# Optimization experiments

Measured on AMD Instinct MI355X. Metric: run time of the kernel, lower is better.

## Reference

```python
import jax, jax.numpy as jnp
import numpy as np

N = 100000   # nodes
E = 1600000  # edges
EL = 1000000 # label edges
F = 64       # node_features (== LSTM hidden)
S = 64       # second_features
C = 32       # num_classes


def setup_inputs() -> dict:
    key = jax.random.key(0)
    ks = jax.random.split(key, 11)
    sc = 0.05
    return {
        "x": jax.random.normal(ks[0], (N, F), jnp.float32),
        "edge_index": jax.random.randint(ks[1], (2, E), 0, N, jnp.int32),
        "edge_label_index": jax.random.randint(ks[2], (2, EL), 0, N, jnp.int32),
        "W_ih": jax.random.normal(ks[3], (4 * F, F), jnp.float32) * sc,
        "W_hh": jax.random.normal(ks[4], (4 * F, F), jnp.float32) * sc,
        "b_ih": jax.random.normal(ks[5], (4 * F,), jnp.float32) * sc,
        "b_hh": jax.random.normal(ks[6], (4 * F,), jnp.float32) * sc,
        "W1": jax.random.normal(ks[7], (F, S), jnp.float32) * sc,
        "b1": jnp.zeros((S,), jnp.float32),
        "W2": jax.random.normal(ks[8], (S, C), jnp.float32) * sc,
        "b2": jnp.zeros((C,), jnp.float32),
    }


def lstm_step(x, W_ih, W_hh, b_ih, b_hh):
    # seq_len == 1, h0 = c0 = 0, so W_hh contributes nothing but both biases apply.
    gates = x @ W_ih.T + b_ih + b_hh          # [N, 4F], PyTorch gate order i,f,g,o
    i, f, g, o = jnp.split(gates, 4, axis=-1)
    c = jax.nn.sigmoid(i) * jnp.tanh(g)
    return jax.nn.sigmoid(o) * jnp.tanh(c)    # [N, F]


def gcn_conv(h, W, b, row, col, n):
    # PyG GCNConv default: add self-loops, symmetric normalization.
    hw = h @ W                                 # [n, out]
    loop = jnp.arange(n, dtype=row.dtype)
    row_sl = jnp.concatenate([row, loop])
    col_sl = jnp.concatenate([col, loop])
    deg = jax.ops.segment_sum(jnp.ones_like(col_sl, jnp.float32), col_sl, num_segments=n)
    dinv = jnp.where(deg > 0, jax.lax.rsqrt(deg), 0.0)
    norm = dinv[row_sl] * dinv[col_sl]         # [E+n]
    msgs = hw[row_sl] * norm[:, None]          # gather + scale
    out = jax.ops.segment_sum(msgs, col_sl, num_segments=n)  # scatter-add
    return out + b


def reference(x, edge_index, edge_label_index, W_ih, W_hh, b_ih, b_hh, W1, b1, W2, b2):
    n = x.shape[0]
    row, col = edge_index[0], edge_index[1]
    h = lstm_step(x, W_ih, W_hh, b_ih, b_hh)
    h = jax.nn.relu(gcn_conv(h, W1, b1, row, col, n))
    z = gcn_conv(h, W2, b2, row, col, n)       # [n, C]
    src = z[edge_label_index[0]]
    dst = z[edge_label_index[1]]
    return jnp.sum(src * dst, axis=-1)         # [EL]
```

## Files before the change

kernel.cpp:

```cpp
#include <hip/hip_runtime.h>
#include <hip/hip_bf16.h>
#include <hip/hip_fp16.h>
#include <math.h>
#include <stdint.h>

#define NBSH 9
#define CH   4096

typedef _Float16 h2v  __attribute__((ext_vector_type(2)));
typedef _Float16 half8 __attribute__((ext_vector_type(8)));
typedef float    f32x4 __attribute__((ext_vector_type(4)));

__device__ __forceinline__ float fdot2_(unsigned a, unsigned b, float c) {
    return __builtin_amdgcn_fdot2(__builtin_bit_cast(h2v, a),
                                  __builtin_bit_cast(h2v, b), c, false);
}

__device__ __forceinline__ float2 h2f2_(unsigned u) {
    return __half22float2(__builtin_bit_cast(__half2, u));
}

__device__ __forceinline__ float fast_sigmoid(float x) {
    float t = __expf(x);
    return 1.0f - __builtin_amdgcn_rcpf(1.0f + t);
}
__device__ __forceinline__ float fast_tanh(float x) {
    float t = __expf(2.0f * x);
    return 1.0f - 2.0f * __builtin_amdgcn_rcpf(1.0f + t);
}

__global__ __launch_bounds__(256) void k_trh(
    const float* __restrict__ Wih, const float* __restrict__ W1,
    const float* __restrict__ bih, const float* __restrict__ bhh,
    uint4* __restrict__ B1tab, uint4* __restrict__ B2tab,
    float* __restrict__ bsum,
    const int* __restrict__ col, int* __restrict__ bdeg, int E, int nbuck)
{
    if (blockIdx.x < 9) {
        int t = blockIdx.x * 256 + threadIdx.x;
        if (t < 1536) {
            int e = t >> 6, l = t & 63;
            int tt = e >> 1, kh = e & 1;
            int gate = tt >> 2, tj = tt & 3;
            int j = 16 * tj + (l & 15);
            int rowb = (gate == 0) ? j : (gate == 1) ? (128 + j) : (192 + j);
            int kbase = kh * 32 + 8 * (l >> 4);
            _Float16 v[8];
#pragma unroll
            for (int jj = 0; jj < 8; jj++)
                v[jj] = (_Float16)Wih[rowb * 64 + kbase + jj];
            B1tab[t] = *reinterpret_cast<uint4*>(v);
        } else if (t < 2048) {
            int u = t - 1536;
            int e = u >> 6, l = u & 63;
            int tt = e >> 1, kh = e & 1;
            int s = 16 * tt + (l & 15);
            int kbase = kh * 32 + 8 * (l >> 4);
            _Float16 v[8];
#pragma unroll
            for (int jj = 0; jj < 8; jj++)
                v[jj] = (_Float16)W1[(kbase + jj) * 64 + s];
            B2tab[u] = *reinterpret_cast<uint4*>(v);
        } else if (t < 2240) {
            int c = t - 2048;
            int gate = c >> 6, j = c & 63;
            int rowb = (gate == 0) ? j : (gate == 1) ? (128 + j) : (192 + j);
            bsum[c] = bih[rowb] + bhh[rowb];
        }
        return;
    }
    __shared__ int cnt[256];
    cnt[threadIdx.x] = 0;
    __syncthreads();
    int base = (blockIdx.x - 9) * CH;
    int end  = base + CH; if (end > E) end = E;
    for (int t = base + (int)threadIdx.x; t < end; t += 256)
        atomicAdd(&cnt[col[t] >> NBSH], 1);
    __syncthreads();
    if ((int)threadIdx.x < nbuck && cnt[threadIdx.x] > 0)
        atomicAdd(&bdeg[threadIdx.x], cnt[threadIdx.x]);
}

__global__ __launch_bounds__(256) void k_bscan(const int* __restrict__ bdeg,
        int* __restrict__ boff, int* __restrict__ gcur, int nbuck, int E) {
    __shared__ int tmp[256];
    int tid = threadIdx.x;
    int v = (tid < nbuck) ? bdeg[tid] : 0;
    tmp[tid] = v;
    __syncthreads();
#pragma unroll
    for (int s = 1; s < 256; s <<= 1) {
        int t = (tid >= s) ? tmp[tid - s] : 0;
        __syncthreads();
        tmp[tid] += t;
        __syncthreads();
    }
    if (tid < nbuck) {
        int o = tmp[tid] - v;
        boff[tid] = o;
        gcur[tid * 16] = o;
    }
    if (tid == 0) boff[nbuck] = E;
}

__global__ __launch_bounds__(256) void k_binl(
    const int* __restrict__ row, const int* __restrict__ col,
    int* __restrict__ gcur, int2* __restrict__ ebuf, int E, int nbuck,
    int eblocks,
    const float* __restrict__ x, const uint4* __restrict__ B1tab,
    const uint4* __restrict__ B2tab, const float* __restrict__ bsum,
    __half* __restrict__ hw1, int n)
{
    __shared__ int pool[9216];
    if ((int)blockIdx.x < eblocks) {
        int* cnt  = pool;
        int* lofs = pool + 256;
        int* gbase = pool + 512;
        int* cur2 = pool + 768;
        int2* stage = (int2*)(pool + 1024);
        int tid  = threadIdx.x;
        int base = blockIdx.x * CH;
        int ned  = E - base; if (ned > CH) ned = CH;

        cnt[tid] = 0;
        __syncthreads();

        int r[16], c[16], b[16];
#pragma unroll
        for (int i = 0; i < 16; i++) {
            int idx = i * 256 + tid;
            if (idx < ned) {
                r[i] = row[base + idx];
                c[i] = col[base + idx];
                b[i] = c[i] >> NBSH;
                atomicAdd(&cnt[b[i]], 1);
            } else { r[i] = 0; c[i] = 0; b[i] = -1; }
        }
        __syncthreads();

        int v = cnt[tid];
        lofs[tid] = v;
        __syncthreads();
#pragma unroll
        for (int s = 1; s < 256; s <<= 1) {
            int t = (tid >= s) ? lofs[tid - s] : 0;
            __syncthreads();
            lofs[tid] += t;
            __syncthreads();
        }
        int excl = lofs[tid] - v;
        __syncthreads();
        lofs[tid] = excl;
        cur2[tid] = excl;
        if (tid < nbuck && v > 0)
            gbase[tid] = atomicAdd(&gcur[tid * 16], v);
        __syncthreads();

#pragma unroll
        for (int i = 0; i < 16; i++) {
            if (b[i] >= 0) {
                int p = atomicAdd(&cur2[b[i]], 1);
                stage[p] = make_int2(r[i], c[i]);
            }
        }
        __syncthreads();

        for (int i = tid; i < ned; i += 256) {
            int2 rc = stage[i];
            int bb = rc.y >> NBSH;
            ebuf[gbase[bb] + (i - lofs[bb])] = rc;
        }
        return;
    }

    _Float16* hsp = (_Float16*)pool;
    int wv   = threadIdx.x >> 6;
    int lane = threadIdx.x & 63;
    int nbase = (((int)blockIdx.x - eblocks) * 4 + wv) * 16;
    if (nbase >= n) return;
    int m16 = lane & 15, q = lane >> 4;
    _Float16* hs = hsp + wv * 1152;

    int node = nbase + m16; if (node >= n) node = n - 1;
    const float* xr = x + (size_t)node * 64 + 8 * q;
    half8 a0, a1;
#pragma unroll
    for (int jj = 0; jj < 8; jj++) a0[jj] = (_Float16)xr[jj];
#pragma unroll
    for (int jj = 0; jj < 8; jj++) a1[jj] = (_Float16)xr[32 + jj];

    f32x4 c1[12];
#pragma unroll
    for (int t = 0; t < 12; t++) {
        f32x4 acc = {0.f, 0.f, 0.f, 0.f};
        half8 b0 = __builtin_bit_cast(half8, B1tab[(t * 2 + 0) * 64 + lane]);
        half8 b1 = __builtin_bit_cast(half8, B1tab[(t * 2 + 1) * 64 + lane]);
        acc = __builtin_amdgcn_mfma_f32_16x16x32_f16(a0, b0, acc, 0, 0, 0);
        acc = __builtin_amdgcn_mfma_f32_16x16x32_f16(a1, b1, acc, 0, 0, 0);
        c1[t] = acc;
    }

#pragma unroll
    for (int tj = 0; tj < 4; tj++) {
        int j = 16 * tj + m16;
        float bi = bsum[j], bg = bsum[64 + j], bo = bsum[128 + j];
#pragma unroll
        for (int r = 0; r < 4; r++) {
            float gi = c1[tj][r]     + bi;
            float gg = c1[4 + tj][r] + bg;
            float go = c1[8 + tj][r] + bo;
            float cc = fast_sigmoid(gi) * fast_tanh(gg);
            float h  = fast_sigmoid(go) * fast_tanh(cc);
            hs[(q * 4 + r) * 72 + j] = (_Float16)h;
        }
    }

    half8 a20 = __builtin_bit_cast(half8,
        *reinterpret_cast<const uint4*>(&hs[m16 * 72 + 8 * q]));
    half8 a21 = __builtin_bit_cast(half8,
        *reinterpret_cast<const uint4*>(&hs[m16 * 72 + 32 + 8 * q]));

    f32x4 c2[4];
#pragma unroll
    for (int t = 0; t < 4; t++) {
        f32x4 acc = {0.f, 0.f, 0.f, 0.f};
        half8 b0 = __builtin_bit_cast(half8, B2tab[(t * 2 + 0) * 64 + lane]);
        half8 b1 = __builtin_bit_cast(half8, B2tab[(t * 2 + 1) * 64 + lane]);
        acc = __builtin_amdgcn_mfma_f32_16x16x32_f16(a20, b0, acc, 0, 0, 0);
        acc = __builtin_amdgcn_mfma_f32_16x16x32_f16(a21, b1, acc, 0, 0, 0);
        c2[t] = acc;
    }

#pragma unroll
    for (int t = 0; t < 4; t++) {
#pragma unroll
        for (int r = 0; r < 4; r++) {
            int nd = nbase + q * 4 + r;
            if (nd < n)
                hw1[(size_t)nd * 64 + 16 * t + m16] = __float2half(c2[t][r]);
        }
    }
}

__global__ __launch_bounds__(512) void k_csr(
    const int2* __restrict__ ebuf, const int* __restrict__ boff,
    int* __restrict__ off, float* __restrict__ dinv,
    int* __restrict__ nbr, int n, int nbuck, int E)
{
    __shared__ int cnt[512], lofs[512];
    int b   = blockIdx.x;
    int tid = threadIdx.x;
    int c0  = b << NBSH;
    int nn  = n - c0; if (nn > 512) nn = 512; if (nn < 0) nn = 0;
    int lo  = boff[b], hi = boff[b + 1];

    cnt[tid] = 0;
    __syncthreads();
    for (int t = lo + tid; t < hi; t += 512)
        atomicAdd(&cnt[ebuf[t].y & 511], 1);
    __syncthreads();

    int v = cnt[tid];
    lofs[tid] = v;
    __syncthreads();
#pragma unroll
    for (int s = 1; s < 512; s <<= 1) {
        int t = (tid >= s) ? lofs[tid - s] : 0;
        __syncthreads();
        lofs[tid] += t;
        __syncthreads();
    }
    int excl = lofs[tid] - v;
    __syncthreads();

    if (tid < nn) {
        off[c0 + tid]  = lo + excl;
        dinv[c0 + tid] = 1.0f / sqrtf((float)(v + 1));
    }
    if (b == nbuck - 1 && tid == 0) off[n] = E;

    cnt[tid] = excl;
    __syncthreads();
    for (int t = lo + tid; t < hi; t += 512) {
        int2 rc = ebuf[t];
        int p = atomicAdd(&cnt[rc.y & 511], 1);
        nbr[lo + p] = rc.x;
    }
}

__global__ __launch_bounds__(256) void k_pull64(
    const __half* __restrict__ hw, const int* __restrict__ off,
    const int* __restrict__ nbr, const float* __restrict__ dinv,
    const float* __restrict__ b1, __half* __restrict__ h1, int n)
{
    int w    = (blockIdx.x * 256 + threadIdx.x) >> 6;
    int lane = threadIdx.x & 63;
    int quad = lane >> 4;
    int fp   = lane & 15;
    if (w * 4 >= n) return;
    int node = w * 4 + quad;
    bool alive = node < n;
    int s = 0, e = 0;
    if (alive) { s = off[node]; e = off[node + 1]; }

    float s0x=0.f,s0y=0.f,s0z=0.f,s0w=0.f;
    float s1x=0.f,s1y=0.f,s1z=0.f,s1w=0.f;
    float s2x=0.f,s2y=0.f,s2z=0.f,s2w=0.f;
    float s3x=0.f,s3y=0.f,s3z=0.f,s3w=0.f;

    for (int base = s; base < e; base += 16) {
        int t = base + fp;
        int idx = 0; float wv = 0.f;
        if (t < e) { idx = nbr[t]; wv = dinv[idx]; }
        int cnt = e - base; if (cnt > 16) cnt = 16;

        int k = 0;
        for (; k + 4 <= cnt; k += 4) {
            int   r0 = __shfl(idx, k + 0, 16); float w0 = __shfl(wv, k + 0, 16);
            int   r1 = __shfl(idx, k + 1, 16); float w1 = __shfl(wv, k + 1, 16);
            int   r2 = __shfl(idx, k + 2, 16); float w2 = __shfl(wv, k + 2, 16);
            int   r3 = __shfl(idx, k + 3, 16); float w3 = __shfl(wv, k + 3, 16);
            uint2 u0 = reinterpret_cast<const uint2*>(hw + (size_t)r0 * 64)[fp];
            uint2 u1 = reinterpret_cast<const uint2*>(hw + (size_t)r1 * 64)[fp];
            uint2 u2 = reinterpret_cast<const uint2*>(hw + (size_t)r2 * 64)[fp];
            uint2 u3 = reinterpret_cast<const uint2*>(hw + (size_t)r3 * 64)[fp];
            float2 l0 = h2f2_(u0.x), h0 = h2f2_(u0.y);
            float2 l1 = h2f2_(u1.x), h1f = h2f2_(u1.y);
            float2 l2 = h2f2_(u2.x), h2 = h2f2_(u2.y);
            float2 l3 = h2f2_(u3.x), h3 = h2f2_(u3.y);
            s0x = fmaf(l0.x, w0, s0x); s0y = fmaf(l0.y, w0, s0y);
            s0z = fmaf(h0.x, w0, s0z); s0w = fmaf(h0.y, w0, s0w);
            s1x = fmaf(l1.x, w1, s1x); s1y = fmaf(l1.y, w1, s1y);
            s1z = fmaf(h1f.x, w1, s1z); s1w = fmaf(h1f.y, w1, s1w);
            s2x = fmaf(l2.x, w2, s2x); s2y = fmaf(l2.y, w2, s2y);
            s2z = fmaf(h2.x, w2, s2z); s2w = fmaf(h2.y, w2, s2w);
            s3x = fmaf(l3.x, w3, s3x); s3y = fmaf(l3.y, w3, s3y);
            s3z = fmaf(h3.x, w3, s3z); s3w = fmaf(h3.y, w3, s3w);
        }
        for (; k < cnt; k++) {
            int   r0 = __shfl(idx, k, 16);
            float w0 = __shfl(wv, k, 16);
            uint2 u0 = reinterpret_cast<const uint2*>(hw + (size_t)r0 * 64)[fp];
            float2 l0 = h2f2_(u0.x), h0 = h2f2_(u0.y);
            s0x = fmaf(l0.x, w0, s0x); s0y = fmaf(l0.y, w0, s0y);
            s0z = fmaf(h0.x, w0, s0z); s0w = fmaf(h0.y, w0, s0w);
        }
    }

    if (alive) {
        float ax = (s0x + s1x) + (s2x + s3x);
        float ay = (s0y + s1y) + (s2y + s3y);
        float az = (s0z + s1z) + (s2z + s3z);
        float aw = (s0w + s1w) + (s2w + s3w);
        float dc = dinv[node];
        uint2 su = reinterpret_cast<const uint2*>(hw + (size_t)node * 64)[fp];
        float2 sl = h2f2_(su.x), sh = h2f2_(su.y);
        float4 bb = reinterpret_cast<const float4*>(b1)[fp];
        float vx = fmaxf(ax * dc + sl.x * dc * dc + bb.x, 0.0f);
        float vy = fmaxf(ay * dc + sl.y * dc * dc + bb.y, 0.0f);
        float vz = fmaxf(az * dc + sh.x * dc * dc + bb.z, 0.0f);
        float vw = fmaxf(aw * dc + sh.y * dc * dc + bb.w, 0.0f);
        __half2 p0(__float2half(vx), __float2half(vy));
        __half2 p1(__float2half(vz), __float2half(vw));
        uint2 pk = make_uint2(__builtin_bit_cast(unsigned, p0),
                              __builtin_bit_cast(unsigned, p1));
        reinterpret_cast<uint2*>(h1 + (size_t)node * 64)[fp] = pk;
    }
}

__global__ __launch_bounds__(256) void k_pull32(
    const __half* __restrict__ hw, const int* __restrict__ off,
    const int* __restrict__ nbr, const float* __restrict__ dinv,
    const float* __restrict__ b2, __half* __restrict__ z, int n)
{
    int w    = (blockIdx.x * 256 + threadIdx.x) >> 6;
    int lane = threadIdx.x & 63;
    int quad = lane >> 4;
    int fp   = lane & 15;
    if (w * 4 >= n) return;
    int node = w * 4 + quad;
    bool alive = node < n;
    int s = 0, e = 0;
    if (alive) { s = off[node]; e = off[node + 1]; }

    float ax0 = 0.f, ay0 = 0.f, ax1 = 0.f, ay1 = 0.f;
    float ax2 = 0.f, ay2 = 0.f, ax3 = 0.f, ay3 = 0.f;

    for (int base = s; base < e; base += 16) {
        int t = base + fp;
        int idx = 0; float wv = 0.f;
        if (t < e) { idx = nbr[t]; wv = dinv[idx]; }
        int cnt = e - base; if (cnt > 16) cnt = 16;

        int k = 0;
        for (; k + 4 <= cnt; k += 4) {
            int   r0 = __shfl(idx, k + 0, 16); float w0 = __shfl(wv, k + 0, 16);
            int   r1 = __shfl(idx, k + 1, 16); float w1 = __shfl(wv, k + 1, 16);
            int   r2 = __shfl(idx, k + 2, 16); float w2 = __shfl(wv, k + 2, 16);
            int   r3 = __shfl(idx, k + 3, 16); float w3 = __shfl(wv, k + 3, 16);
            unsigned u0 = reinterpret_cast<const unsigned*>(hw + (size_t)r0 * 32)[fp];
            unsigned u1 = reinterpret_cast<const unsigned*>(hw + (size_t)r1 * 32)[fp];
            unsigned u2 = reinterpret_cast<const unsigned*>(hw + (size_t)r2 * 32)[fp];
            unsigned u3 = reinterpret_cast<const unsigned*>(hw + (size_t)r3 * 32)[fp];
            float2 f0 = h2f2_(u0), f1 = h2f2_(u1), f2 = h2f2_(u2), f3 = h2f2_(u3);
            ax0 = fmaf(f0.x, w0, ax0); ay0 = fmaf(f0.y, w0, ay0);
            ax1 = fmaf(f1.x, w1, ax1); ay1 = fmaf(f1.y, w1, ay1);
            ax2 = fmaf(f2.x, w2, ax2); ay2 = fmaf(f2.y, w2, ay2);
            ax3 = fmaf(f3.x, w3, ax3); ay3 = fmaf(f3.y, w3, ay3);
        }
        for (; k < cnt; k++) {
            int   r0 = __shfl(idx, k, 16);
            float w0 = __shfl(wv, k, 16);
            unsigned u0 = reinterpret_cast<const unsigned*>(hw + (size_t)r0 * 32)[fp];
            float2 f0 = h2f2_(u0);
            ax0 = fmaf(f0.x, w0, ax0); ay0 = fmaf(f0.y, w0, ay0);
        }
    }

    if (alive) {
        float ax = (ax0 + ax1) + (ax2 + ax3);
        float ay = (ay0 + ay1) + (ay2 + ay3);
        float dc = dinv[node];
        unsigned su = reinterpret_cast<const unsigned*>(hw + (size_t)node * 32)[fp];
        float2 sf = h2f2_(su);
        float2 bb = reinterpret_cast<const float2*>(b2)[fp];
        float vx = ax * dc + sf.x * dc * dc + bb.x;
        float vy = ay * dc + sf.y * dc * dc + bb.y;
        __half2 pk(__float2half(vx), __float2half(vy));
        reinterpret_cast<__half2*>(z + (size_t)node * 32)[fp] = pk;
    }
}

__global__ __launch_bounds__(128) void k_mm2(
    const __half* __restrict__ h1, const float* __restrict__ W2,
    __half* __restrict__ hw2, int n)
{
    __shared__ float tile[128 * 65];
    int base  = blockIdx.x * 128;
    int nrows = n - base; if (nrows > 128) nrows = 128;

    for (int idx = threadIdx.x; idx < nrows * 32; idx += 128) {
        int r = idx >> 5, c = idx & 31;
        __half2 hv = reinterpret_cast<const __half2*>(h1 + (size_t)(base + r) * 64)[c];
        float2 f = __half22float2(hv);
        tile[r * 65 + 2 * c]     = f.x;
        tile[r * 65 + 2 * c + 1] = f.y;
    }
    __syncthreads();

    int node = base + threadIdx.x;
    if (node >= n) return;

    const float* hrow = &tile[threadIdx.x * 65];
    float acc[32];
#pragma unroll
    for (int s = 0; s < 32; s++) acc[s] = 0.0f;

    for (int k = 0; k < 64; k++) {
        float hk = hrow[k];
        const float* w = W2 + (size_t)k * 32;
#pragma unroll
        for (int s = 0; s < 32; s++) acc[s] = fmaf(hk, w[s], acc[s]);
    }

    uint2* op = reinterpret_cast<uint2*>(hw2 + (size_t)node * 32);
#pragma unroll
    for (int q = 0; q < 8; q++) {
        __half2 lo(__float2half(acc[4*q+0]), __float2half(acc[4*q+1]));
        __half2 hi(__float2half(acc[4*q+2]), __float2half(acc[4*q+3]));
        op[q] = make_uint2(__builtin_bit_cast(unsigned, lo),
                           __builtin_bit_cast(unsigned, hi));
    }
}

__global__ void k_dot(const __half* __restrict__ z, const int* __restrict__ src,
                      const int* __restrict__ dst, float* __restrict__ out, int EL)
{
    int e = blockIdx.x * 256 + threadIdx.x;
    if (e >= EL) return;
    const uint4* a = reinterpret_cast<const uint4*>(z + (size_t)src[e] * 32);
    const uint4* b = reinterpret_cast<const uint4*>(z + (size_t)dst[e] * 32);
    float s = 0.0f;
#pragma unroll
    for (int q = 0; q < 4; q++) {
        uint4 av = a[q], bv = b[q];
        s = fdot2_(av.x, bv.x, s);
        s = fdot2_(av.y, bv.y, s);
        s = fdot2_(av.z, bv.z, s);
        s = fdot2_(av.w, bv.w, s);
    }
    out[e] = s;
}

extern "C" void kernel_launch(void* const* d_in, const int* in_sizes, int n_in,
                              void* d_out, int out_size, void* d_ws, size_t ws_size,
                              hipStream_t stream)
{
    const float* x   = (const float*)d_in[0];
    const int*   ei  = (const int*)d_in[1];
    const int*   eli = (const int*)d_in[2];
    const float* Wih = (const float*)d_in[3];
    const float* bih = (const float*)d_in[5];
    const float* bhh = (const float*)d_in[6];
    const float* W1  = (const float*)d_in[7];
    const float* b1  = (const float*)d_in[8];
    const float* W2  = (const float*)d_in[9];
    const float* b2  = (const float*)d_in[10];

    int n  = in_sizes[0] / 64;
    int E  = in_sizes[1] / 2;
    int EL = in_sizes[2] / 2;

    const int* row  = ei;
    const int* col  = ei + E;
    const int* lsrc = eli;
    const int* ldst = eli + EL;
    float* out = (float*)d_out;

    float*    base  = (float*)d_ws;
    int2*     ebuf  = (int2*)base;
    __half*   hw2h  = (__half*)base;
    float*    p1    = base + (size_t)E * 2;
    __half*   hw1h  = (__half*)p1;
    float*    p2    = p1 + (size_t)n * 32;
    __half*   h1h   = (__half*)p2;
    __half*   zh    = (__half*)p2;
    float*    dinv  = p2 + (size_t)n * 32;
    int*      off   = (int*)(dinv + n);
    int*      nbr   = off + (n + 1);
    uintptr_t pal   = ((uintptr_t)(nbr + E) + 15) & ~(uintptr_t)15;
    uint4*    B1tab = (uint4*)pal;
    uint4*    B2tab = B1tab + 1536;
    float*    bsum  = (float*)(B2tab + 512);
    int*      bdeg  = (int*)(bsum + 192);
    int*      boff  = bdeg + 256;
    int*      gcur  = boff + 257;

    int nbuck   = (n + (1 << NBSH) - 1) >> NBSH;
    int eblocks = (E + CH - 1) / CH;
    int lblocks = (n + 63) / 64;
    dim3 blk(256);

    hipMemsetAsync(bdeg, 0, 256 * sizeof(int), stream);
    k_trh<<<dim3(9 + eblocks), blk, 0, stream>>>(
        Wih, W1, bih, bhh, B1tab, B2tab, bsum, col, bdeg, E, nbuck);
    k_bscan<<<dim3(1), blk, 0, stream>>>(bdeg, boff, gcur, nbuck, E);

    k_binl<<<dim3(eblocks + lblocks), blk, 0, stream>>>(
        row, col, gcur, ebuf, E, nbuck, eblocks,
        x, B1tab, B2tab, bsum, hw1h, n);

    k_csr<<<dim3(nbuck), dim3(512), 0, stream>>>(ebuf, boff, off, dinv, nbr, n, nbuck, E);

    {
        int blocks = (n + 15) / 16;
        k_pull64<<<dim3(blocks), blk, 0, stream>>>(hw1h, off, nbr, dinv, b1, h1h, n);
    }

    k_mm2<<<dim3((n + 127) / 128), dim3(128), 0, stream>>>(h1h, W2, hw2h, n);

    {
        int blocks = (n + 15) / 16;
        k_pull32<<<dim3(blocks), blk, 0, stream>>>(hw2h, off, nbr, dinv, b2, zh, n);
    }

    k_dot<<<dim3((EL + 255) / 256), blk, 0, stream>>>(zh, lsrc, ldst, out, EL);
}
```

Measured before the change: 180.0 us.

## Fuse second GCN linear transform into first aggregation kernel

Result: faster. 167.6 us (-6.9%).

```diff
diff --git a/kernel.cpp b/kernel.cpp
--- a/kernel.cpp
+++ b/kernel.cpp
@@ -31,12 +31,13 @@
 
 __global__ __launch_bounds__(256) void k_trh(
     const float* __restrict__ Wih, const float* __restrict__ W1,
+    const float* __restrict__ W2,
     const float* __restrict__ bih, const float* __restrict__ bhh,
     uint4* __restrict__ B1tab, uint4* __restrict__ B2tab,
-    float* __restrict__ bsum,
+    float* __restrict__ bsum, unsigned* __restrict__ W2P,
     const int* __restrict__ col, int* __restrict__ bdeg, int E, int nbuck)
 {
-    if (blockIdx.x < 9) {
+    if (blockIdx.x < 13) {
         int t = blockIdx.x * 256 + threadIdx.x;
         if (t < 1536) {
             int e = t >> 6, l = t & 63;
@@ -66,13 +67,20 @@
             int gate = c >> 6, j = c & 63;
             int rowb = (gate == 0) ? j : (gate == 1) ? (128 + j) : (192 + j);
             bsum[c] = bih[rowb] + bhh[rowb];
+        } else if (t < 3264) {
+            int u = t - 2240;
+            int kk = u >> 5, s = u & 31;
+            h2v p;
+            p.x = (_Float16)W2[(2 * kk)     * 32 + s];
+            p.y = (_Float16)W2[(2 * kk + 1) * 32 + s];
+            W2P[u] = __builtin_bit_cast(unsigned, p);
         }
         return;
     }
     __shared__ int cnt[256];
     cnt[threadIdx.x] = 0;
     __syncthreads();
-    int base = (blockIdx.x - 9) * CH;
+    int base = (blockIdx.x - 13) * CH;
     int end  = base + CH; if (end > E) end = E;
     for (int t = base + (int)threadIdx.x; t < end; t += 256)
         atomicAdd(&cnt[col[t] >> NBSH], 1);
@@ -288,13 +296,21 @@
     }
 }
 
-__global__ __launch_bounds__(256) void k_pull64(
+__global__ __launch_bounds__(256) void k_pull64mm(
     const __half* __restrict__ hw, const int* __restrict__ off,
     const int* __restrict__ nbr, const float* __restrict__ dinv,
-    const float* __restrict__ b1, __half* __restrict__ h1, int n)
-{
+    const float* __restrict__ b1, const unsigned* __restrict__ W2P,
+    __half* __restrict__ hw2, int n)
+{
+    __shared__ unsigned w2p[1024];
+    __shared__ _Float16 hrow[4][256];
+
+    for (int i = threadIdx.x; i < 1024; i += 256) w2p[i] = W2P[i];
+    __syncthreads();
+
     int w    = (blockIdx.x * 256 + threadIdx.x) >> 6;
     int lane = threadIdx.x & 63;
+    int wv   = threadIdx.x >> 6;
     int quad = lane >> 4;
     int fp   = lane & 15;
     if (w * 4 >= n) return;
@@ -310,16 +326,16 @@
 
     for (int base = s; base < e; base += 16) {
         int t = base + fp;
-        int idx = 0; float wv = 0.f;
-        if (t < e) { idx = nbr[t]; wv = dinv[idx]; }
+        int idx = 0; float wv2 = 0.f;
+        if (t < e) { idx = nbr[t]; wv2 = dinv[idx]; }
         int cnt = e - base; if (cnt > 16) cnt = 16;
 
         int k = 0;
         for (; k + 4 <= cnt; k += 4) {
-            int   r0 = __shfl(idx, k + 0, 16); float w0 = __shfl(wv, k + 0, 16);
-            int   r1 = __shfl(idx, k + 1, 16); float w1 = __shfl(wv, k + 1, 16);
-            int   r2 = __shfl(idx, k + 2, 16); float w2 = __shfl(wv, k + 2, 16);
-            int   r3 = __shfl(idx, k + 3, 16); float w3 = __shfl(wv, k + 3, 16);
+            int   r0 = __shfl(idx, k + 0, 16); float w0 = __shfl(wv2, k + 0, 16);
+            int   r1 = __shfl(idx, k + 1, 16); float w1 = __shfl(wv2, k + 1, 16);
+            int   r2 = __shfl(idx, k + 2, 16); float w2 = __shfl(wv2, k + 2, 16);
+            int   r3 = __shfl(idx, k + 3, 16); float w3 = __shfl(wv2, k + 3, 16);
             uint2 u0 = reinterpret_cast<const uint2*>(hw + (size_t)r0 * 64)[fp];
             uint2 u1 = reinterpret_cast<const uint2*>(hw + (size_t)r1 * 64)[fp];
             uint2 u2 = reinterpret_cast<const uint2*>(hw + (size_t)r2 * 64)[fp];
@@ -339,7 +355,7 @@
         }
         for (; k < cnt; k++) {
             int   r0 = __shfl(idx, k, 16);
-            float w0 = __shfl(wv, k, 16);
+            float w0 = __shfl(wv2, k, 16);
             uint2 u0 = reinterpret_cast<const uint2*>(hw + (size_t)r0 * 64)[fp];
             float2 l0 = h2f2_(u0.x), h0 = h2f2_(u0.y);
             s0x = fmaf(l0.x, w0, s0x); s0y = fmaf(l0.y, w0, s0y);
@@ -347,13 +363,14 @@
         }
     }
 
-    if (alive) {
+    {
         float ax = (s0x + s1x) + (s2x + s3x);
         float ay = (s0y + s1y) + (s2y + s3y);
         float az = (s0z + s1z) + (s2z + s3z);
         float aw = (s0w + s1w) + (s2w + s3w);
-        float dc = dinv[node];
-        uint2 su = reinterpret_cast<const uint2*>(hw + (size_t)node * 64)[fp];
+        float dc = alive ? dinv[node] : 0.f;
+        uint2 su = alive ? reinterpret_cast<const uint2*>(hw + (size_t)node * 64)[fp]
+                         : make_uint2(0u, 0u);
         float2 sl = h2f2_(su.x), sh = h2f2_(su.y);
         float4 bb = reinterpret_cast<const float4*>(b1)[fp];
         float vx = fmaxf(ax * dc + sl.x * dc * dc + bb.x, 0.0f);
@@ -364,7 +381,20 @@
         __half2 p1(__float2half(vz), __float2half(vw));
         uint2 pk = make_uint2(__builtin_bit_cast(unsigned, p0),
                               __builtin_bit_cast(unsigned, p1));
-        reinterpret_cast<uint2*>(h1 + (size_t)node * 64)[fp] = pk;
+        *reinterpret_cast<uint2*>(&hrow[wv][quad * 64 + 4 * fp]) = pk;
+    }
+
+    float acc0 = 0.f, acc1 = 0.f;
+#pragma unroll 8
+    for (int kk = 0; kk < 32; kk++) {
+        unsigned a = *reinterpret_cast<const unsigned*>(&hrow[wv][quad * 64 + 2 * kk]);
+        uint2 wp = *reinterpret_cast<const uint2*>(&w2p[kk * 32 + 2 * fp]);
+        acc0 = fdot2_(a, wp.x, acc0);
+        acc1 = fdot2_(a, wp.y, acc1);
+    }
+    if (alive) {
+        __half2 pk(__float2half(acc0), __float2half(acc1));
+        reinterpret_cast<__half2*>(hw2 + (size_t)node * 32)[fp] = pk;
     }
 }
 
@@ -431,48 +461,6 @@
     }
 }
 
-__global__ __launch_bounds__(128) void k_mm2(
-    const __half* __restrict__ h1, const float* __restrict__ W2,
-    __half* __restrict__ hw2, int n)
-{
-    __shared__ float tile[128 * 65];
-    int base  = blockIdx.x * 128;
-    int nrows = n - base; if (nrows > 128) nrows = 128;
-
-    for (int idx = threadIdx.x; idx < nrows * 32; idx += 128) {
-        int r = idx >> 5, c = idx & 31;
-        __half2 hv = reinterpret_cast<const __half2*>(h1 + (size_t)(base + r) * 64)[c];
-        float2 f = __half22float2(hv);
-        tile[r * 65 + 2 * c]     = f.x;
-        tile[r * 65 + 2 * c + 1] = f.y;
-    }
-    __syncthreads();
-
-    int node = base + threadIdx.x;
-    if (node >= n) return;
-
-    const float* hrow = &tile[threadIdx.x * 65];
-    float acc[32];
-#pragma unroll
-    for (int s = 0; s < 32; s++) acc[s] = 0.0f;
-
-    for (int k = 0; k < 64; k++) {
-        float hk = hrow[k];
-        const float* w = W2 + (size_t)k * 32;
-#pragma unroll
-        for (int s = 0; s < 32; s++) acc[s] = fmaf(hk, w[s], acc[s]);
-    }
-
-    uint2* op = reinterpret_cast<uint2*>(hw2 + (size_t)node * 32);
-#pragma unroll
-    for (int q = 0; q < 8; q++) {
-        __half2 lo(__float2half(acc[4*q+0]), __float2half(acc[4*q+1]));
-        __half2 hi(__float2half(acc[4*q+2]), __float2half(acc[4*q+3]));
-        op[q] = make_uint2(__builtin_bit_cast(unsigned, lo),
-                           __builtin_bit_cast(unsigned, hi));
-    }
-}
-
 __global__ void k_dot(const __half* __restrict__ z, const int* __restrict__ src,
                       const int* __restrict__ dst, float* __restrict__ out, int EL)
 {
@@ -519,20 +507,20 @@
 
     float*    base  = (float*)d_ws;
     int2*     ebuf  = (int2*)base;
-    __half*   hw2h  = (__half*)base;
     float*    p1    = base + (size_t)E * 2;
     __half*   hw1h  = (__half*)p1;
+    __half*   zh    = (__half*)p1;
     float*    p2    = p1 + (size_t)n * 32;
-    __half*   h1h   = (__half*)p2;
-    __half*   zh    = (__half*)p2;
-    float*    dinv  = p2 + (size_t)n * 32;
+    __half*   hw2h  = (__half*)p2;
+    float*    dinv  = p2 + (size_t)n * 16;
     int*      off   = (int*)(dinv + n);
     int*      nbr   = off + (n + 1);
     uintptr_t pal   = ((uintptr_t)(nbr + E) + 15) & ~(uintptr_t)15;
     uint4*    B1tab = (uint4*)pal;
     uint4*    B2tab = B1tab + 1536;
     float*    bsum  = (float*)(B2tab + 512);
-    int*      bdeg  = (int*)(bsum + 192);
+    unsigned* W2P   = (unsigned*)(bsum + 192);
+    int*      bdeg  = (int*)(W2P + 1024);
     int*      boff  = bdeg + 256;
     int*      gcur  = boff + 257;
 
@@ -542,8 +530,8 @@
     dim3 blk(256);
 
     hipMemsetAsync(bdeg, 0, 256 * sizeof(int), stream);
-    k_trh<<<dim3(9 + eblocks), blk, 0, stream>>>(
-        Wih, W1, bih, bhh, B1tab, B2tab, bsum, col, bdeg, E, nbuck);
+    k_trh<<<dim3(13 + eblocks), blk, 0, stream>>>(
+        Wih, W1, W2, bih, bhh, B1tab, B2tab, bsum, W2P, col, bdeg, E, nbuck);
     k_bscan<<<dim3(1), blk, 0, stream>>>(bdeg, boff, gcur, nbuck, E);
 
     k_binl<<<dim3(eblocks + lblocks), blk, 0, stream>>>(
@@ -554,10 +542,9 @@
 
     {
         int blocks = (n + 15) / 16;
-        k_pull64<<<dim3(blocks), blk, 0, stream>>>(hw1h, off, nbr, dinv, b1, h1h, n);
-    }
-
-    k_mm2<<<dim3((n + 127) / 128), dim3(128), 0, stream>>>(h1h, W2, hw2h, n);
+        k_pull64mm<<<dim3(blocks), blk, 0, stream>>>(
+            hw1h, off, nbr, dinv, b1, W2P, hw2h, n);
+    }
 
     {
         int blocks = (n + 15) / 16;
```
